# Optimization experiments

Hardware: AMD Instinct MI355X
Metric: run time of the kernel (lower is better)

Reference implementation:

```python
import jax, jax.numpy as jnp
import numpy as np

B = 32; H = 56; W = 56; C = 384; WS = 7; SHIFT = 3; NH = 12; HID = 1536; RANK = 192
N = WS * WS
NWIN = (H // WS) * (W // WS)


def _rel_index():
    coords = np.stack(np.meshgrid(np.arange(WS), np.arange(WS), indexing='ij')).reshape(2, -1)
    rel = (coords[:, :, None] - coords[:, None, :]).transpose(1, 2, 0)
    rel[..., 0] += WS - 1
    rel[..., 1] += WS - 1
    rel[..., 0] *= 2 * WS - 1
    return jnp.asarray(rel.sum(-1).reshape(-1))  # (N*N,) int


def _attn_mask():
    img = np.zeros((H, W))
    cnt = 0
    sls = (slice(0, -WS), slice(-WS, -SHIFT), slice(-SHIFT, None))
    for hs in sls:
        for ws_ in sls:
            img[hs, ws_] = cnt
            cnt += 1
    mw = img.reshape(H // WS, WS, W // WS, WS).transpose(0, 2, 1, 3).reshape(-1, N)
    am = mw[:, None, :] - mw[:, :, None]
    return jnp.asarray(np.where(am != 0, -100.0, 0.0).astype(np.float32))  # (nW,N,N)


REL_IDX = _rel_index()
ATTN_MASK = _attn_mask()


def _ln(x, g, b):
    m = x.mean(-1, keepdims=True)
    v = ((x - m) ** 2).mean(-1, keepdims=True)
    return (x - m) / jnp.sqrt(v + 1e-5) * g + b


def _flin(x, v, u, b):
    # FactorizedLinear: x @ V^T @ U^T + b
    return (x @ v.T) @ u.T + b


def setup_inputs() -> dict:
    key = jax.random.key(0)
    ks = jax.random.split(key, 12)
    def n(k, shape, s):
        return jax.random.normal(k, shape, jnp.float32) * s
    return {
        'x': jax.random.normal(ks[0], (B, H * W, C), jnp.float32),
        'norm1_g': jnp.ones((C,), jnp.float32), 'norm1_b': jnp.zeros((C,), jnp.float32),
        'rpb_table': n(ks[1], ((2 * WS - 1) ** 2, NH), 0.02),
        'qkv_v': n(ks[2], (RANK, C), 0.05), 'qkv_u': n(ks[3], (3 * C, RANK), 0.05),
        'qkv_b': jnp.zeros((3 * C,), jnp.float32),
        'proj_v': n(ks[4], (RANK, C), 0.05), 'proj_u': n(ks[5], (C, RANK), 0.05),
        'proj_b': jnp.zeros((C,), jnp.float32),
        'norm2_g': jnp.ones((C,), jnp.float32), 'norm2_b': jnp.zeros((C,), jnp.float32),
        'fc1_v': n(ks[6], (RANK, C), 0.05), 'fc1_u': n(ks[7], (HID, RANK), 0.05),
        'fc1_b': jnp.zeros((HID,), jnp.float32),
        'fc2_v': n(ks[8], (RANK, HID), 0.05), 'fc2_u': n(ks[9], (C, RANK), 0.05),
        'fc2_b': jnp.zeros((C,), jnp.float32),
    }


def reference(x, norm1_g, norm1_b, rpb_table, qkv_v, qkv_u, qkv_b,
              proj_v, proj_u, proj_b, norm2_g, norm2_b,
              fc1_v, fc1_u, fc1_b, fc2_v, fc2_u, fc2_b):
    hd = C // NH
    scale = hd ** -0.5
    shortcut = x
    y = _ln(x, norm1_g, norm1_b).reshape(B, H, W, C)
    y = jnp.roll(y, (-SHIFT, -SHIFT), axis=(1, 2))  # cyclic shift
    # window partition -> (B*nW, N, C)
    y = y.reshape(B, H // WS, WS, W // WS, WS, C).transpose(0, 1, 3, 2, 4, 5).reshape(-1, N, C)
    qkv = _flin(y, qkv_v, qkv_u, qkv_b).reshape(-1, N, 3, NH, hd).transpose(2, 0, 3, 1, 4)
    q, k, v = qkv[0] * scale, qkv[1], qkv[2]  # (B*nW, NH, N, hd)
    attn = jnp.einsum('bhnd,bhmd->bhnm', q, k)
    rpb = rpb_table[REL_IDX].reshape(N, N, NH).transpose(2, 0, 1)  # (NH,N,N)
    attn = attn + rpb[None]
    attn = attn.reshape(B, NWIN, NH, N, N) + ATTN_MASK[None, :, None]
    attn = jax.nn.softmax(attn, axis=-1).reshape(-1, NH, N, N)
    o = jnp.einsum('bhnm,bhmd->bhnd', attn, v).transpose(0, 2, 1, 3).reshape(-1, N, C)
    o = _flin(o, proj_v, proj_u, proj_b)
    # window reverse + reverse shift
    o = o.reshape(B, H // WS, W // WS, WS, WS, C).transpose(0, 1, 3, 2, 4, 5).reshape(B, H, W, C)
    o = jnp.roll(o, (SHIFT, SHIFT), axis=(1, 2)).reshape(B, H * W, C)
    x = shortcut + o
    z = _ln(x, norm2_g, norm2_b)
    z = jax.nn.gelu(_flin(z, fc1_v, fc1_u, fc1_b), approximate=False)
    z = _flin(z, fc2_v, fc2_u, fc2_b)
    return x + z
```

## Files before the change

### kernel.cpp

```cpp
#include <hip/hip_runtime.h>
#include <hip/hip_bf16.h>

using bf16 = __hip_bfloat16;
typedef __bf16 bf16x8 __attribute__((ext_vector_type(8)));
typedef float f32x4 __attribute__((ext_vector_type(4)));

#define MROWS 100352

__device__ __forceinline__ void async16(void* l, const void* g) {
    void* gg = const_cast<void*>(g);
    __builtin_amdgcn_global_load_lds((__attribute__((address_space(1))) void*)gg,
                                     (__attribute__((address_space(3))) void*)l, 16, 0, 0);
}

__device__ __forceinline__ float gelu_f(float x) {
    float u = 0.7978845608028654f * (x + 0.044715f * x * x * x);
    float e = __expf(2.0f * u);
    float t = 1.0f - 2.0f / (e + 1.0f);
    return 0.5f * x * (1.0f + t);
}

__device__ __forceinline__ unsigned short bfu(float x) {
    bf16 b = __float2bfloat16(x);
    union { bf16 b; unsigned short u; } c; c.b = b; return c.u;
}

struct Cvt8 { const float* s[8]; bf16* d[8]; int n[8]; };

__global__ __launch_bounds__(256) void cvt8_k(Cvt8 c) {
    int seg = blockIdx.y;
    int i4 = (blockIdx.x * 256 + threadIdx.x) * 4;
    if (i4 < c.n[seg]) {
        float4 v = *(const float4*)(c.s[seg] + i4);
        bf16* d = c.d[seg] + i4;
        d[0] = __float2bfloat16(v.x);
        d[1] = __float2bfloat16(v.y);
        d[2] = __float2bfloat16(v.z);
        d[3] = __float2bfloat16(v.w);
    }
}

__global__ __launch_bounds__(256) void ln1_window_k(const float* __restrict__ x,
                                                    const float* __restrict__ g,
                                                    const float* __restrict__ bta,
                                                    bf16* __restrict__ ywin) {
    int wrow = blockIdx.x * 4 + (threadIdx.x >> 6);
    int lane = threadIdx.x & 63;
    int tok = wrow % 49, win = wrow / 49;
    int i = tok / 7, j = tok % 7;
    int wwi = win & 7, whi = (win >> 3) & 7, bi = win >> 6;
    int hs = (whi * 7 + i + 3) % 56;
    int ws_ = (wwi * 7 + j + 3) % 56;
    const float* xr = x + ((size_t)bi * 3136 + (size_t)hs * 56 + ws_) * 384;
    float v[6]; float s = 0.f, s2 = 0.f;
#pragma unroll
    for (int u = 0; u < 6; ++u) { float t = xr[lane + 64 * u]; v[u] = t; s += t; s2 += t * t; }
#pragma unroll
    for (int d = 1; d < 64; d <<= 1) { s += __shfl_xor(s, d); s2 += __shfl_xor(s2, d); }
    float mean = s * (1.0f / 384.0f);
    float var = s2 * (1.0f / 384.0f) - mean * mean;
    float rstd = rsqrtf(var + 1e-5f);
    bf16* yr = ywin + (size_t)wrow * 384;
#pragma unroll
    for (int u = 0; u < 6; ++u) {
        int c = lane + 64 * u;
        yr[c] = __float2bfloat16((v[u] - mean) * rstd * g[c] + bta[c]);
    }
}

__global__ __launch_bounds__(256) void resid_ln2_k(const float* __restrict__ x,
                                                   const bf16* __restrict__ proj,
                                                   const float* __restrict__ g,
                                                   const float* __restrict__ bta,
                                                   float* __restrict__ x2,
                                                   bf16* __restrict__ z) {
    int row = blockIdx.x * 4 + (threadIdx.x >> 6);
    int lane = threadIdx.x & 63;
    int bi = row / 3136; int hw = row % 3136;
    int h = hw / 56, w = hw % 56;
    int h2 = (h + 53) % 56, w2 = (w + 53) % 56;
    int prow = ((bi * 8 + h2 / 7) * 8 + w2 / 7) * 49 + (h2 % 7) * 7 + (w2 % 7);
    const float* xr = x + (size_t)row * 384;
    const bf16* pr = proj + (size_t)prow * 384;
    float* x2r = x2 + (size_t)row * 384;
    float v[6]; float s = 0.f, s2 = 0.f;
#pragma unroll
    for (int u = 0; u < 6; ++u) {
        int c = lane + 64 * u;
        float t = xr[c] + __bfloat162float(pr[c]);
        v[u] = t; s += t; s2 += t * t;
        x2r[c] = t;
    }
#pragma unroll
    for (int d = 1; d < 64; d <<= 1) { s += __shfl_xor(s, d); s2 += __shfl_xor(s2, d); }
    float mean = s * (1.0f / 384.0f);
    float var = s2 * (1.0f / 384.0f) - mean * mean;
    float rstd = rsqrtf(var + 1e-5f);
    bf16* zr = z + (size_t)row * 384;
#pragma unroll
    for (int u = 0; u < 6; ++u) {
        int c = lane + 64 * u;
        zr[c] = __float2bfloat16((v[u] - mean) * rstd * g[c] + bta[c]);
    }
}

__global__ __launch_bounds__(256) void attn_mfma_k(const bf16* __restrict__ qkv,
                                                   const float* __restrict__ rpbt,
                                                   bf16* __restrict__ o) {
    __shared__ __align__(16) __bf16 vt_s[4][32 * 72];
    __shared__ __align__(16) __bf16 p_s[4][32 * 72];
    __shared__ float rpb_sh[676];
    const int win = blockIdx.x;
    const int r = blockIdx.y;
    const int wave = threadIdx.x >> 6, lane = threadIdx.x & 63;
    const int lo = lane & 15, hi = lane >> 4;
    const int whi = (win >> 3) & 7, wwi = win & 7;
    const bool bH = (whi == 7), bW = (wwi == 7);
    const bool boundary = bH || bW;
    __bf16* vt_w = vt_s[wave];
    __bf16* p_w = p_s[wave];
    const int h = r * 4 + wave;
    const bf16* qbase = qkv + (size_t)win * 49 * 1152 + h * 32;
    bf16x8 zf = {};

    for (int idx = threadIdx.x; idx < 676; idx += 256)
        rpb_sh[idx] = rpbt[(idx >> 2) * 12 + r * 4 + (idx & 3)];
    __syncthreads();

    {
        int m = lane;
        bf16x8 vrow[4];
#pragma unroll
        for (int d8 = 0; d8 < 4; ++d8)
            vrow[d8] = (m < 49) ? *(const bf16x8*)(qbase + (size_t)m * 1152 + 768 + d8 * 8) : zf;
#pragma unroll
        for (int d8 = 0; d8 < 4; ++d8)
#pragma unroll
            for (int e = 0; e < 8; ++e)
                vt_w[(d8 * 8 + e) * 72 + m] = vrow[d8][e];
    }
    bf16x8 aq[4], bk[4];
    const int kq = hi * 8;
#pragma unroll
    for (int ta = 0; ta < 4; ++ta) {
        int n = ta * 16 + lo;
        aq[ta] = (n < 49) ? *(const bf16x8*)(qbase + (size_t)n * 1152 + kq) : zf;
        bk[ta] = (n < 49) ? *(const bf16x8*)(qbase + (size_t)n * 1152 + 384 + kq) : zf;
    }
    f32x4 acc[4][4] = {};
#pragma unroll
    for (int ta = 0; ta < 4; ++ta)
#pragma unroll
        for (int tb = 0; tb < 4; ++tb)
            acc[ta][tb] = __builtin_amdgcn_mfma_f32_16x16x32_bf16(aq[ta], bk[tb], acc[ta][tb], 0, 0, 0);
    int i2[4], j2[4], rm[4];
#pragma unroll
    for (int tb = 0; tb < 4; ++tb) {
        int m = tb * 16 + lo;
        int mm = m < 49 ? m : 0;
        i2[tb] = mm / 7; j2[tb] = mm % 7;
        rm[tb] = (bH ? (i2[tb] < 4 ? 1 : 2) : 0) * 3 + (bW ? (j2[tb] < 4 ? 1 : 2) : 0);
    }
#pragma unroll
    for (int ta = 0; ta < 4; ++ta) {
#pragma unroll
        for (int j = 0; j < 4; ++j) {
            int n = ta * 16 + hi * 4 + j;
            int nn = n < 49 ? n : 0;
            int i1 = nn / 7, j1 = nn % 7;
            int rn = (bH ? (i1 < 4 ? 1 : 2) : 0) * 3 + (bW ? (j1 < 4 ? 1 : 2) : 0);
#pragma unroll
            for (int tb = 0; tb < 4; ++tb) {
                int m = tb * 16 + lo;
                float v;
                if (n < 49 && m < 49) {
                    v = acc[ta][tb][j] * 0.17677669529663687f
                        + rpb_sh[((i1 - i2[tb] + 6) * 13 + (j1 - j2[tb] + 6)) * 4 + wave];
                    if (boundary && rn != rm[tb]) v -= 100.0f;
                } else {
                    v = -1e30f;
                }
                acc[ta][tb][j] = v;
            }
        }
    }
    bf16x8 vb[2][2];
#pragma unroll
    for (int kb = 0; kb < 2; ++kb)
#pragma unroll
        for (int tb = 0; tb < 2; ++tb)
            vb[kb][tb] = *(const bf16x8*)(vt_w + (tb * 16 + lo) * 72 + kb * 32 + hi * 8);

    f32x4 oacc[4][2] = {};
#pragma unroll
    for (int half = 0; half < 2; ++half) {
#pragma unroll
        for (int tq = 0; tq < 2; ++tq) {
            int ta = half * 2 + tq;
#pragma unroll
            for (int j = 0; j < 4; ++j) {
                float mx = fmaxf(fmaxf(acc[ta][0][j], acc[ta][1][j]),
                                 fmaxf(acc[ta][2][j], acc[ta][3][j]));
                mx = fmaxf(mx, __shfl_xor(mx, 1));
                mx = fmaxf(mx, __shfl_xor(mx, 2));
                mx = fmaxf(mx, __shfl_xor(mx, 4));
                mx = fmaxf(mx, __shfl_xor(mx, 8));
                float e0 = __expf(acc[ta][0][j] - mx);
                float e1 = __expf(acc[ta][1][j] - mx);
                float e2 = __expf(acc[ta][2][j] - mx);
                float e3 = __expf(acc[ta][3][j] - mx);
                float sm = e0 + e1 + e2 + e3;
                sm += __shfl_xor(sm, 1);
                sm += __shfl_xor(sm, 2);
                sm += __shfl_xor(sm, 4);
                sm += __shfl_xor(sm, 8);
                float inv = 1.0f / sm;
                int nl = tq * 16 + hi * 4 + j;
                p_w[nl * 72 + lo]      = (__bf16)(e0 * inv);
                p_w[nl * 72 + 16 + lo] = (__bf16)(e1 * inv);
                p_w[nl * 72 + 32 + lo] = (__bf16)(e2 * inv);
                p_w[nl * 72 + 48 + lo] = (__bf16)(e3 * inv);
            }
        }
#pragma unroll
        for (int kb = 0; kb < 2; ++kb) {
#pragma unroll
            for (int tq = 0; tq < 2; ++tq) {
                bf16x8 pa = *(const bf16x8*)(p_w + (tq * 16 + lo) * 72 + kb * 32 + hi * 8);
#pragma unroll
                for (int tb = 0; tb < 2; ++tb)
                    oacc[half * 2 + tq][tb] =
                        __builtin_amdgcn_mfma_f32_16x16x32_bf16(pa, vb[kb][tb], oacc[half * 2 + tq][tb], 0, 0, 0);
            }
        }
    }
    bf16* obase = o + (size_t)win * 49 * 384 + h * 32;
#pragma unroll
    for (int ta = 0; ta < 4; ++ta) {
#pragma unroll
        for (int j = 0; j < 4; ++j) {
            int n = ta * 16 + hi * 4 + j;
            if (n < 49) {
#pragma unroll
                for (int tb = 0; tb < 2; ++tb)
                    obase[(size_t)n * 384 + tb * 16 + lo] = __float2bfloat16(oacc[ta][tb][j]);
            }
        }
    }
}

template <int K, int EPI>
__global__ __launch_bounds__(256) void gemm_bt(const bf16* __restrict__ A,
                                               const bf16* __restrict__ W,
                                               const float* __restrict__ bias,
                                               void* __restrict__ Cout,
                                               int N) {
    __shared__ __align__(16) bf16 lds_a[128 * 64];
    __shared__ __align__(16) bf16 lds_b[64 * 64];
    const int t = threadIdx.x;
    const int wave = t >> 6, lane = t & 63;
    const int gdx = gridDim.x;
    int flat = blockIdx.y * gdx + blockIdx.x;
    int q = (gdx * gridDim.y) >> 3;
    int work = (flat & 7) * q + (flat >> 3);
    const int n0 = (work % gdx) * 64, m0 = (work / gdx) * 128;
    const int wm = wave >> 1, wn = wave & 1;
    const int fr = lane & 15, hi = lane >> 4;
    f32x4 acc[4][2] = {};
    for (int kt = 0; kt < K; kt += 64) {
        if (kt > 0) __syncthreads();
#pragma unroll
        for (int i = 0; i < 4; ++i) {
            int u = i * 256 + t;
            int row = u >> 3, slot = u & 7;
            int gslot = slot ^ (row & 7);
            async16((char*)lds_a + u * 16, A + (size_t)(m0 + row) * K + kt + gslot * 8);
        }
#pragma unroll
        for (int i = 0; i < 2; ++i) {
            int u = i * 256 + t;
            int row = u >> 3, slot = u & 7;
            int gslot = slot ^ (row & 7);
            async16((char*)lds_b + u * 16, W + (size_t)(n0 + row) * K + kt + gslot * 8);
        }
        __syncthreads();
#pragma unroll
        for (int ks = 0; ks < 2; ++ks) {
            bf16x8 af[4], bfr[2];
#pragma unroll
            for (int mi = 0; mi < 4; ++mi) {
                int row = wm * 64 + mi * 16 + fr;
                int slot = (ks * 4 + hi) ^ (row & 7);
                af[mi] = *(const bf16x8*)((const char*)lds_a + row * 128 + slot * 16);
            }
#pragma unroll
            for (int ni = 0; ni < 2; ++ni) {
                int row = wn * 32 + ni * 16 + fr;
                int slot = (ks * 4 + hi) ^ (row & 7);
                bfr[ni] = *(const bf16x8*)((const char*)lds_b + row * 128 + slot * 16);
            }
#pragma unroll
            for (int mi = 0; mi < 4; ++mi)
#pragma unroll
                for (int ni = 0; ni < 2; ++ni)
                    acc[mi][ni] = __builtin_amdgcn_mfma_f32_16x16x32_bf16(bfr[ni], af[mi], acc[mi][ni], 0, 0, 0);
        }
    }
    const int rq4 = hi * 4;
#pragma unroll
    for (int mi = 0; mi < 4; ++mi) {
        int m = m0 + wm * 64 + mi * 16 + fr;
        size_t rowb = (size_t)m * N;
#pragma unroll
        for (int ni = 0; ni < 2; ++ni) {
            int nb = n0 + wn * 32 + ni * 16 + rq4;
            float v0 = acc[mi][ni][0], v1 = acc[mi][ni][1];
            float v2 = acc[mi][ni][2], v3 = acc[mi][ni][3];
            if (bias) {
                float4 b4 = *(const float4*)(bias + nb);
                v0 += b4.x; v1 += b4.y; v2 += b4.z; v3 += b4.w;
            }
            if (EPI == 1) { v0 = gelu_f(v0); v1 = gelu_f(v1); v2 = gelu_f(v2); v3 = gelu_f(v3); }
            if (EPI == 2) {
                float4* p = (float4*)((float*)Cout + rowb + nb);
                float4 o = *p;
                o.x += v0; o.y += v1; o.z += v2; o.w += v3;
                *p = o;
            } else {
                uint2 st;
                st.x = (unsigned)bfu(v0) | ((unsigned)bfu(v1) << 16);
                st.y = (unsigned)bfu(v2) | ((unsigned)bfu(v3) << 16);
                *(uint2*)((bf16*)Cout + rowb + nb) = st;
            }
        }
    }
}

extern "C" void kernel_launch(void* const* d_in, const int* in_sizes, int n_in,
                              void* d_out, int out_size, void* d_ws, size_t ws_size,
                              hipStream_t stream) {
    const float* x      = (const float*)d_in[0];
    const float* n1g    = (const float*)d_in[1];
    const float* n1b    = (const float*)d_in[2];
    const float* rpbt   = (const float*)d_in[3];
    const float* qkv_v  = (const float*)d_in[4];
    const float* qkv_u  = (const float*)d_in[5];
    const float* qkv_b  = (const float*)d_in[6];
    const float* proj_v = (const float*)d_in[7];
    const float* proj_u = (const float*)d_in[8];
    const float* proj_b = (const float*)d_in[9];
    const float* n2g    = (const float*)d_in[10];
    const float* n2b    = (const float*)d_in[11];
    const float* fc1_v  = (const float*)d_in[12];
    const float* fc1_u  = (const float*)d_in[13];
    const float* fc1_b  = (const float*)d_in[14];
    const float* fc2_v  = (const float*)d_in[15];
    const float* fc2_u  = (const float*)d_in[16];
    const float* fc2_b  = (const float*)d_in[17];

    char* ws = (char*)d_ws;
    bf16* wb = (bf16*)ws;
    bf16* w_qkv_v  = wb;
    bf16* w_qkv_u  = wb + 73728;
    bf16* w_proj_v = wb + 294912;
    bf16* w_proj_u = wb + 368640;
    bf16* w_fc1_v  = wb + 442368;
    bf16* w_fc1_u  = wb + 516096;
    bf16* w_fc2_v  = wb + 811008;
    bf16* w_fc2_u  = wb + 1105920;
    size_t off = (size_t)4 << 20;
    bf16* R1 = (bf16*)(ws + off); off += (size_t)MROWS * 1536 * 2;
    bf16* R2 = (bf16*)(ws + off); off += (size_t)MROWS * 384 * 2;
    bf16* R3 = (bf16*)(ws + off);
    float* out = (float*)d_out;

    Cvt8 c;
    c.s[0] = qkv_v;  c.d[0] = w_qkv_v;  c.n[0] = 73728;
    c.s[1] = qkv_u;  c.d[1] = w_qkv_u;  c.n[1] = 221184;
    c.s[2] = proj_v; c.d[2] = w_proj_v; c.n[2] = 73728;
    c.s[3] = proj_u; c.d[3] = w_proj_u; c.n[3] = 73728;
    c.s[4] = fc1_v;  c.d[4] = w_fc1_v;  c.n[4] = 73728;
    c.s[5] = fc1_u;  c.d[5] = w_fc1_u;  c.n[5] = 294912;
    c.s[6] = fc2_v;  c.d[6] = w_fc2_v;  c.n[6] = 294912;
    c.s[7] = fc2_u;  c.d[7] = w_fc2_u;  c.n[7] = 73728;
    cvt8_k<<<dim3(288, 8), 256, 0, stream>>>(c);

    ln1_window_k<<<MROWS / 4, 256, 0, stream>>>(x, n1g, n1b, R2);
    gemm_bt<384, 0><<<dim3(3, 784), 256, 0, stream>>>(R2, w_qkv_v, nullptr, R3, 192);
    gemm_bt<192, 0><<<dim3(18, 784), 256, 0, stream>>>(R3, w_qkv_u, qkv_b, R1, 1152);
    attn_mfma_k<<<dim3(2048, 3), 256, 0, stream>>>(R1, rpbt, R2);
    gemm_bt<384, 0><<<dim3(3, 784), 256, 0, stream>>>(R2, w_proj_v, nullptr, R3, 192);
    gemm_bt<192, 0><<<dim3(6, 784), 256, 0, stream>>>(R3, w_proj_u, proj_b, R1, 384);
    resid_ln2_k<<<MROWS / 4, 256, 0, stream>>>(x, R1, n2g, n2b, out, R2);
    gemm_bt<384, 0><<<dim3(3, 784), 256, 0, stream>>>(R2, w_fc1_v, nullptr, R3, 192);
    gemm_bt<192, 1><<<dim3(24, 784), 256, 0, stream>>>(R3, w_fc1_u, fc1_b, R1, 1536);
    gemm_bt<1536, 0><<<dim3(3, 784), 256, 0, stream>>>(R1, w_fc2_v, nullptr, R3, 192);
    gemm_bt<192, 2><<<dim3(6, 784), 256, 0, stream>>>(R3, w_fc2_u, fc2_b, out, 384);
}
```

Before: 900.5 us.

## Widen GEMM tiles to 64 columns per wave and cover full rank width

The GEMM kernel is generalized so that each wave computes a 64x64 output tile, with a configurable number of waves along N. The rank-192 down-projections now use a 128x192 block with 384 threads, so each A row-block is loaded once instead of three times. The up-projections use 128x128 blocks. This cuts redundant A-tile global loads and raises MFMA work per LDS fragment read, at the cost of more accumulator registers and fewer blocks in the grid.

```diff
diff --git a/kernel.cpp b/kernel.cpp
--- a/kernel.cpp
+++ b/kernel.cpp
@@ -249,44 +249,50 @@
     }
 }
 
-template <int K, int EPI>
-__global__ __launch_bounds__(256) void gemm_bt(const bf16* __restrict__ A,
-                                               const bf16* __restrict__ W,
-                                               const float* __restrict__ bias,
-                                               void* __restrict__ Cout,
-                                               int N) {
+template <int K, int NWN, int EPI>
+__global__ __launch_bounds__(NWN * 128) void gemm_w64(const bf16* __restrict__ A,
+                                                      const bf16* __restrict__ W,
+                                                      const float* __restrict__ bias,
+                                                      void* __restrict__ Cout,
+                                                      int N) {
+    constexpr int T = NWN * 128;
+    constexpr int BN = NWN * 64;
     __shared__ __align__(16) bf16 lds_a[128 * 64];
-    __shared__ __align__(16) bf16 lds_b[64 * 64];
+    __shared__ __align__(16) bf16 lds_b[BN * 64];
     const int t = threadIdx.x;
     const int wave = t >> 6, lane = t & 63;
+    const int wm = wave / NWN, wn = wave % NWN;
+    const int fr = lane & 15, hi = lane >> 4;
     const int gdx = gridDim.x;
     int flat = blockIdx.y * gdx + blockIdx.x;
     int q = (gdx * gridDim.y) >> 3;
     int work = (flat & 7) * q + (flat >> 3);
-    const int n0 = (work % gdx) * 64, m0 = (work / gdx) * 128;
-    const int wm = wave >> 1, wn = wave & 1;
-    const int fr = lane & 15, hi = lane >> 4;
-    f32x4 acc[4][2] = {};
+    const int n0 = (work % gdx) * BN, m0 = (work / gdx) * 128;
+    f32x4 acc[4][4] = {};
     for (int kt = 0; kt < K; kt += 64) {
         if (kt > 0) __syncthreads();
 #pragma unroll
-        for (int i = 0; i < 4; ++i) {
-            int u = i * 256 + t;
-            int row = u >> 3, slot = u & 7;
-            int gslot = slot ^ (row & 7);
-            async16((char*)lds_a + u * 16, A + (size_t)(m0 + row) * K + kt + gslot * 8);
-        }
-#pragma unroll
-        for (int i = 0; i < 2; ++i) {
-            int u = i * 256 + t;
-            int row = u >> 3, slot = u & 7;
-            int gslot = slot ^ (row & 7);
-            async16((char*)lds_b + u * 16, W + (size_t)(n0 + row) * K + kt + gslot * 8);
+        for (int i = 0; i < 1024; i += T) {
+            int u = i + t;
+            if (u < 1024) {
+                int row = u >> 3, slot = u & 7;
+                int gslot = slot ^ (row & 7);
+                async16((char*)lds_a + u * 16, A + (size_t)(m0 + row) * K + kt + gslot * 8);
+            }
+        }
+#pragma unroll
+        for (int i = 0; i < BN * 8; i += T) {
+            int u = i + t;
+            if (u < BN * 8) {
+                int row = u >> 3, slot = u & 7;
+                int gslot = slot ^ (row & 7);
+                async16((char*)lds_b + u * 16, W + (size_t)(n0 + row) * K + kt + gslot * 8);
+            }
         }
         __syncthreads();
 #pragma unroll
         for (int ks = 0; ks < 2; ++ks) {
-            bf16x8 af[4], bfr[2];
+            bf16x8 af[4], bfr[4];
 #pragma unroll
             for (int mi = 0; mi < 4; ++mi) {
                 int row = wm * 64 + mi * 16 + fr;
@@ -294,26 +300,25 @@
                 af[mi] = *(const bf16x8*)((const char*)lds_a + row * 128 + slot * 16);
             }
 #pragma unroll
-            for (int ni = 0; ni < 2; ++ni) {
-                int row = wn * 32 + ni * 16 + fr;
+            for (int ni = 0; ni < 4; ++ni) {
+                int row = wn * 64 + ni * 16 + fr;
                 int slot = (ks * 4 + hi) ^ (row & 7);
                 bfr[ni] = *(const bf16x8*)((const char*)lds_b + row * 128 + slot * 16);
             }
 #pragma unroll
             for (int mi = 0; mi < 4; ++mi)
 #pragma unroll
-                for (int ni = 0; ni < 2; ++ni)
+                for (int ni = 0; ni < 4; ++ni)
                     acc[mi][ni] = __builtin_amdgcn_mfma_f32_16x16x32_bf16(bfr[ni], af[mi], acc[mi][ni], 0, 0, 0);
         }
     }
-    const int rq4 = hi * 4;
 #pragma unroll
     for (int mi = 0; mi < 4; ++mi) {
         int m = m0 + wm * 64 + mi * 16 + fr;
         size_t rowb = (size_t)m * N;
 #pragma unroll
-        for (int ni = 0; ni < 2; ++ni) {
-            int nb = n0 + wn * 32 + ni * 16 + rq4;
+        for (int ni = 0; ni < 4; ++ni) {
+            int nb = n0 + wn * 64 + ni * 16 + hi * 4;
             float v0 = acc[mi][ni][0], v1 = acc[mi][ni][1];
             float v2 = acc[mi][ni][2], v3 = acc[mi][ni][3];
             if (bias) {
@@ -386,14 +391,14 @@
     cvt8_k<<<dim3(288, 8), 256, 0, stream>>>(c);
 
     ln1_window_k<<<MROWS / 4, 256, 0, stream>>>(x, n1g, n1b, R2);
-    gemm_bt<384, 0><<<dim3(3, 784), 256, 0, stream>>>(R2, w_qkv_v, nullptr, R3, 192);
-    gemm_bt<192, 0><<<dim3(18, 784), 256, 0, stream>>>(R3, w_qkv_u, qkv_b, R1, 1152);
+    gemm_w64<384, 3, 0><<<dim3(1, 784), 384, 0, stream>>>(R2, w_qkv_v, nullptr, R3, 192);
+    gemm_w64<192, 2, 0><<<dim3(9, 784), 256, 0, stream>>>(R3, w_qkv_u, qkv_b, R1, 1152);
     attn_mfma_k<<<dim3(2048, 3), 256, 0, stream>>>(R1, rpbt, R2);
-    gemm_bt<384, 0><<<dim3(3, 784), 256, 0, stream>>>(R2, w_proj_v, nullptr, R3, 192);
-    gemm_bt<192, 0><<<dim3(6, 784), 256, 0, stream>>>(R3, w_proj_u, proj_b, R1, 384);
+    gemm_w64<384, 3, 0><<<dim3(1, 784), 384, 0, stream>>>(R2, w_proj_v, nullptr, R3, 192);
+    gemm_w64<192, 2, 0><<<dim3(3, 784), 256, 0, stream>>>(R3, w_proj_u, proj_b, R1, 384);
     resid_ln2_k<<<MROWS / 4, 256, 0, stream>>>(x, R1, n2g, n2b, out, R2);
-    gemm_bt<384, 0><<<dim3(3, 784), 256, 0, stream>>>(R2, w_fc1_v, nullptr, R3, 192);
-    gemm_bt<192, 1><<<dim3(24, 784), 256, 0, stream>>>(R3, w_fc1_u, fc1_b, R1, 1536);
-    gemm_bt<1536, 0><<<dim3(3, 784), 256, 0, stream>>>(R1, w_fc2_v, nullptr, R3, 192);
-    gemm_bt<192, 2><<<dim3(6, 784), 256, 0, stream>>>(R3, w_fc2_u, fc2_b, out, 384);
-}
+    gemm_w64<384, 3, 0><<<dim3(1, 784), 384, 0, stream>>>(R2, w_fc1_v, nullptr, R3, 192);
+    gemm_w64<192, 2, 1><<<dim3(12, 784), 256, 0, stream>>>(R3, w_fc1_u, fc1_b, R1, 1536);
+    gemm_w64<1536, 3, 0><<<dim3(1, 784), 384, 0, stream>>>(R1, w_fc2_v, nullptr, R3, 192);
+    gemm_w64<192, 2, 2><<<dim3(3, 784), 256, 0, stream>>>(R3, w_fc2_u, fc2_b, out, 384);
+}
```

New measurement: 1.011 ms. 1.12x slower.

## Add persistent-B GEMM for K=192 up-projections with register-resident weights

Applied to the files above, without the earlier changes.

Adds a new GEMM kernel for the K=192 factorized up-projections. Each workgroup keeps its 128-column weight slice in registers and loops over eight 64-row A tiles, double-buffering them in LDS through async global-to-LDS loads with an XOR swizzle. Work is remapped across XCDs so neighbouring tiles land on the same die. This removes repeated weight loads per tile and overlaps A loads with MFMA work, at the cost of higher register pressure and fewer workgroups (grid shrinks fourfold in M).

```diff
diff --git a/kernel.cpp b/kernel.cpp
--- a/kernel.cpp
+++ b/kernel.cpp
@@ -336,6 +336,102 @@
     }
 }
 
+template <int N, int EPI>
+__global__ __launch_bounds__(256) void gemm_pb(const bf16* __restrict__ A,
+                                               const bf16* __restrict__ W,
+                                               const float* __restrict__ bias,
+                                               void* __restrict__ Cout) {
+    constexpr int K = 192;
+    constexpr int MT = 8;
+    __shared__ __align__(16) bf16 lds_a[2][64 * 192];
+    const int t = threadIdx.x;
+    const int wv = t >> 6, lane = t & 63;
+    const int fr = lane & 15, hi = lane >> 4;
+    const int gdx = gridDim.x;
+    int nwg = gdx * gridDim.y;
+    int flat = blockIdx.y * gdx + blockIdx.x;
+    int q = nwg >> 3, r = nwg & 7;
+    int xcd = flat & 7, sub = flat >> 3;
+    int work = (xcd < r ? xcd * (q + 1) : r * (q + 1) + (xcd - r) * q) + sub;
+    const int n0 = (work % gdx) * 128;
+    const int mstrip = (work / gdx) * (MT * 64);
+
+    bf16x8 breg[6][2];
+#pragma unroll
+    for (int kk = 0; kk < 6; ++kk)
+#pragma unroll
+        for (int nn = 0; nn < 2; ++nn)
+            breg[kk][nn] = *(const bf16x8*)(W + (size_t)(n0 + wv * 32 + nn * 16 + fr) * K + kk * 32 + hi * 8);
+
+    bf16* cur = (bf16*)lds_a[0];
+    bf16* nxt = (bf16*)lds_a[1];
+#pragma unroll
+    for (int i = 0; i < 6; ++i) {
+        int u = i * 256 + t;
+        int row = u / 24, slot = u % 24;
+        int gslot = slot ^ (row & 7);
+        async16((char*)cur + u * 16, A + (size_t)(mstrip + row) * K + gslot * 8);
+    }
+    __syncthreads();
+    for (int mt = 0; mt < MT; ++mt) {
+        if (mt + 1 < MT) {
+#pragma unroll
+            for (int i = 0; i < 6; ++i) {
+                int u = i * 256 + t;
+                int row = u / 24, slot = u % 24;
+                int gslot = slot ^ (row & 7);
+                async16((char*)nxt + u * 16,
+                        A + (size_t)(mstrip + (mt + 1) * 64 + row) * K + gslot * 8);
+            }
+        }
+        f32x4 acc[4][2] = {};
+#pragma unroll
+        for (int kk = 0; kk < 6; ++kk) {
+            bf16x8 af[4];
+#pragma unroll
+            for (int mi = 0; mi < 4; ++mi) {
+                int row = mi * 16 + fr;
+                int slot = (kk * 4 + hi) ^ (row & 7);
+                af[mi] = *(const bf16x8*)((const char*)cur + row * 384 + slot * 16);
+            }
+#pragma unroll
+            for (int mi = 0; mi < 4; ++mi)
+#pragma unroll
+                for (int nn = 0; nn < 2; ++nn)
+                    acc[mi][nn] = __builtin_amdgcn_mfma_f32_16x16x32_bf16(breg[kk][nn], af[mi], acc[mi][nn], 0, 0, 0);
+        }
+#pragma unroll
+        for (int mi = 0; mi < 4; ++mi) {
+            int m = mstrip + mt * 64 + mi * 16 + fr;
+            size_t rowb = (size_t)m * N;
+#pragma unroll
+            for (int nn = 0; nn < 2; ++nn) {
+                int nb = n0 + wv * 32 + nn * 16 + hi * 4;
+                float v0 = acc[mi][nn][0], v1 = acc[mi][nn][1];
+                float v2 = acc[mi][nn][2], v3 = acc[mi][nn][3];
+                if (bias) {
+                    float4 b4 = *(const float4*)(bias + nb);
+                    v0 += b4.x; v1 += b4.y; v2 += b4.z; v3 += b4.w;
+                }
+                if (EPI == 1) { v0 = gelu_f(v0); v1 = gelu_f(v1); v2 = gelu_f(v2); v3 = gelu_f(v3); }
+                if (EPI == 2) {
+                    float4* p = (float4*)((float*)Cout + rowb + nb);
+                    float4 o = *p;
+                    o.x += v0; o.y += v1; o.z += v2; o.w += v3;
+                    *p = o;
+                } else {
+                    uint2 st;
+                    st.x = (unsigned)bfu(v0) | ((unsigned)bfu(v1) << 16);
+                    st.y = (unsigned)bfu(v2) | ((unsigned)bfu(v3) << 16);
+                    *(uint2*)((bf16*)Cout + rowb + nb) = st;
+                }
+            }
+        }
+        __syncthreads();
+        bf16* tmp = cur; cur = nxt; nxt = tmp;
+    }
+}
+
 extern "C" void kernel_launch(void* const* d_in, const int* in_sizes, int n_in,
                               void* d_out, int out_size, void* d_ws, size_t ws_size,
                               hipStream_t stream) {
@@ -387,13 +483,13 @@
 
     ln1_window_k<<<MROWS / 4, 256, 0, stream>>>(x, n1g, n1b, R2);
     gemm_bt<384, 0><<<dim3(3, 784), 256, 0, stream>>>(R2, w_qkv_v, nullptr, R3, 192);
-    gemm_bt<192, 0><<<dim3(18, 784), 256, 0, stream>>>(R3, w_qkv_u, qkv_b, R1, 1152);
+    gemm_pb<1152, 0><<<dim3(9, 196), 256, 0, stream>>>(R3, w_qkv_u, qkv_b, R1);
     attn_mfma_k<<<dim3(2048, 3), 256, 0, stream>>>(R1, rpbt, R2);
     gemm_bt<384, 0><<<dim3(3, 784), 256, 0, stream>>>(R2, w_proj_v, nullptr, R3, 192);
-    gemm_bt<192, 0><<<dim3(6, 784), 256, 0, stream>>>(R3, w_proj_u, proj_b, R1, 384);
+    gemm_pb<384, 0><<<dim3(3, 196), 256, 0, stream>>>(R3, w_proj_u, proj_b, R1);
     resid_ln2_k<<<MROWS / 4, 256, 0, stream>>>(x, R1, n2g, n2b, out, R2);
     gemm_bt<384, 0><<<dim3(3, 784), 256, 0, stream>>>(R2, w_fc1_v, nullptr, R3, 192);
-    gemm_bt<192, 1><<<dim3(24, 784), 256, 0, stream>>>(R3, w_fc1_u, fc1_b, R1, 1536);
+    gemm_pb<1536, 1><<<dim3(12, 196), 256, 0, stream>>>(R3, w_fc1_u, fc1_b, R1);
     gemm_bt<1536, 0><<<dim3(3, 784), 256, 0, stream>>>(R1, w_fc2_v, nullptr, R3, 192);
-    gemm_bt<192, 2><<<dim3(6, 784), 256, 0, stream>>>(R3, w_fc2_u, fc2_b, out, 384);
-}
+    gemm_pb<384, 2><<<dim3(3, 196), 256, 0, stream>>>(R3, w_fc2_u, fc2_b, out);
+}
```

New measurement: 926.4 us. 2.9% more time.

## Precompute attention bias+mask tiles per window type; simplify GEMM load addressing

Applied to the files above, without the earlier changes.

Adds a small kernel that precomputes, for each of the four window boundary types and twelve heads, the relative-position bias plus shift mask laid out in MFMA accumulator order. The attention kernel then reads one float4 per row group instead of computing indices, gathering from LDS and applying masks, which also removes an LDS table and a block barrier. Separately, the GEMM hoists its async-load address math out of the k loop and adds a minimum-occupancy launch bound of 6. The new 192 KB bias buffer is read from global/L2 by every attention block.

```diff
diff --git a/kernel.cpp b/kernel.cpp
--- a/kernel.cpp
+++ b/kernel.cpp
@@ -37,6 +37,37 @@
         d[1] = __float2bfloat16(v.y);
         d[2] = __float2bfloat16(v.z);
         d[3] = __float2bfloat16(v.w);
+    }
+}
+
+__global__ __launch_bounds__(256) void bias_pre_k(const float* __restrict__ rpbt,
+                                                  float* __restrict__ biasf) {
+    int wt = blockIdx.x / 12, h = blockIdx.x % 12;
+    int t = threadIdx.x;
+    int lane = t >> 2, tb = t & 3;
+    int hi = lane >> 4, lo = lane & 15;
+    int m = tb * 16 + lo;
+    bool bH = (wt & 2) != 0, bW = (wt & 1) != 0;
+    float* outb = biasf + (size_t)blockIdx.x * 4096;
+    int mm = m < 49 ? m : 0;
+    int i2 = mm / 7, j2 = mm % 7;
+    int rm = (bH ? (i2 < 4 ? 1 : 2) : 0) * 3 + (bW ? (j2 < 4 ? 1 : 2) : 0);
+#pragma unroll
+    for (int ta = 0; ta < 4; ++ta) {
+#pragma unroll
+        for (int j = 0; j < 4; ++j) {
+            int n = ta * 16 + hi * 4 + j;
+            float v;
+            if (n < 49 && m < 49) {
+                int i1 = n / 7, j1 = n % 7;
+                int rn = (bH ? (i1 < 4 ? 1 : 2) : 0) * 3 + (bW ? (j1 < 4 ? 1 : 2) : 0);
+                v = rpbt[((i1 - i2 + 6) * 13 + (j1 - j2 + 6)) * 12 + h];
+                if (rn != rm) v -= 100.0f;
+            } else {
+                v = -1e30f;
+            }
+            outb[(ta * 4 + j) * 256 + t] = v;
+        }
     }
 }
 
@@ -105,27 +136,22 @@
 }
 
 __global__ __launch_bounds__(256) void attn_mfma_k(const bf16* __restrict__ qkv,
-                                                   const float* __restrict__ rpbt,
+                                                   const float* __restrict__ biasf,
                                                    bf16* __restrict__ o) {
     __shared__ __align__(16) __bf16 vt_s[4][32 * 72];
     __shared__ __align__(16) __bf16 p_s[4][32 * 72];
-    __shared__ float rpb_sh[676];
     const int win = blockIdx.x;
     const int r = blockIdx.y;
     const int wave = threadIdx.x >> 6, lane = threadIdx.x & 63;
     const int lo = lane & 15, hi = lane >> 4;
     const int whi = (win >> 3) & 7, wwi = win & 7;
-    const bool bH = (whi == 7), bW = (wwi == 7);
-    const bool boundary = bH || bW;
+    const int wt = ((whi == 7) ? 2 : 0) + ((wwi == 7) ? 1 : 0);
     __bf16* vt_w = vt_s[wave];
     __bf16* p_w = p_s[wave];
     const int h = r * 4 + wave;
     const bf16* qbase = qkv + (size_t)win * 49 * 1152 + h * 32;
+    const float* btile = biasf + (size_t)(wt * 12 + h) * 4096;
     bf16x8 zf = {};
-
-    for (int idx = threadIdx.x; idx < 676; idx += 256)
-        rpb_sh[idx] = rpbt[(idx >> 2) * 12 + r * 4 + (idx & 3)];
-    __syncthreads();
 
     {
         int m = lane;
@@ -153,35 +179,15 @@
 #pragma unroll
         for (int tb = 0; tb < 4; ++tb)
             acc[ta][tb] = __builtin_amdgcn_mfma_f32_16x16x32_bf16(aq[ta], bk[tb], acc[ta][tb], 0, 0, 0);
-    int i2[4], j2[4], rm[4];
-#pragma unroll
-    for (int tb = 0; tb < 4; ++tb) {
-        int m = tb * 16 + lo;
-        int mm = m < 49 ? m : 0;
-        i2[tb] = mm / 7; j2[tb] = mm % 7;
-        rm[tb] = (bH ? (i2[tb] < 4 ? 1 : 2) : 0) * 3 + (bW ? (j2[tb] < 4 ? 1 : 2) : 0);
-    }
 #pragma unroll
     for (int ta = 0; ta < 4; ++ta) {
 #pragma unroll
         for (int j = 0; j < 4; ++j) {
-            int n = ta * 16 + hi * 4 + j;
-            int nn = n < 49 ? n : 0;
-            int i1 = nn / 7, j1 = nn % 7;
-            int rn = (bH ? (i1 < 4 ? 1 : 2) : 0) * 3 + (bW ? (j1 < 4 ? 1 : 2) : 0);
-#pragma unroll
-            for (int tb = 0; tb < 4; ++tb) {
-                int m = tb * 16 + lo;
-                float v;
-                if (n < 49 && m < 49) {
-                    v = acc[ta][tb][j] * 0.17677669529663687f
-                        + rpb_sh[((i1 - i2[tb] + 6) * 13 + (j1 - j2[tb] + 6)) * 4 + wave];
-                    if (boundary && rn != rm[tb]) v -= 100.0f;
-                } else {
-                    v = -1e30f;
-                }
-                acc[ta][tb][j] = v;
-            }
+            float4 b4 = *(const float4*)(btile + (ta * 4 + j) * 256 + lane * 4);
+            acc[ta][0][j] = fmaf(acc[ta][0][j], 0.17677669529663687f, b4.x);
+            acc[ta][1][j] = fmaf(acc[ta][1][j], 0.17677669529663687f, b4.y);
+            acc[ta][2][j] = fmaf(acc[ta][2][j], 0.17677669529663687f, b4.z);
+            acc[ta][3][j] = fmaf(acc[ta][3][j], 0.17677669529663687f, b4.w);
         }
     }
     bf16x8 vb[2][2];
@@ -250,11 +256,11 @@
 }
 
 template <int K, int EPI>
-__global__ __launch_bounds__(256) void gemm_bt(const bf16* __restrict__ A,
-                                               const bf16* __restrict__ W,
-                                               const float* __restrict__ bias,
-                                               void* __restrict__ Cout,
-                                               int N) {
+__global__ __launch_bounds__(256, 6) void gemm_bt(const bf16* __restrict__ A,
+                                                  const bf16* __restrict__ W,
+                                                  const float* __restrict__ bias,
+                                                  void* __restrict__ Cout,
+                                                  int N) {
     __shared__ __align__(16) bf16 lds_a[128 * 64];
     __shared__ __align__(16) bf16 lds_b[64 * 64];
     const int t = threadIdx.x;
@@ -266,23 +272,21 @@
     const int n0 = (work % gdx) * 64, m0 = (work / gdx) * 128;
     const int wm = wave >> 1, wn = wave & 1;
     const int fr = lane & 15, hi = lane >> 4;
+    const int srow = t >> 3;
+    const int gslot = (t & 7) ^ (srow & 7);
+    const bf16* abase = A + (size_t)(m0 + srow) * K + gslot * 8;
+    const bf16* bbase = W + (size_t)(n0 + srow) * K + gslot * 8;
+    char* la = (char*)lds_a + t * 16;
+    char* lb = (char*)lds_b + t * 16;
     f32x4 acc[4][2] = {};
     for (int kt = 0; kt < K; kt += 64) {
         if (kt > 0) __syncthreads();
 #pragma unroll
-        for (int i = 0; i < 4; ++i) {
-            int u = i * 256 + t;
-            int row = u >> 3, slot = u & 7;
-            int gslot = slot ^ (row & 7);
-            async16((char*)lds_a + u * 16, A + (size_t)(m0 + row) * K + kt + gslot * 8);
-        }
-#pragma unroll
-        for (int i = 0; i < 2; ++i) {
-            int u = i * 256 + t;
-            int row = u >> 3, slot = u & 7;
-            int gslot = slot ^ (row & 7);
-            async16((char*)lds_b + u * 16, W + (size_t)(n0 + row) * K + kt + gslot * 8);
-        }
+        for (int i = 0; i < 4; ++i)
+            async16(la + i * 4096, abase + (size_t)i * 32 * K + kt);
+#pragma unroll
+        for (int i = 0; i < 2; ++i)
+            async16(lb + i * 4096, bbase + (size_t)i * 32 * K + kt);
         __syncthreads();
 #pragma unroll
         for (int ks = 0; ks < 2; ++ks) {
@@ -368,6 +372,7 @@
     bf16* w_fc1_u  = wb + 516096;
     bf16* w_fc2_v  = wb + 811008;
     bf16* w_fc2_u  = wb + 1105920;
+    float* biasf   = (float*)(ws + 3145728);
     size_t off = (size_t)4 << 20;
     bf16* R1 = (bf16*)(ws + off); off += (size_t)MROWS * 1536 * 2;
     bf16* R2 = (bf16*)(ws + off); off += (size_t)MROWS * 384 * 2;
@@ -384,11 +389,12 @@
     c.s[6] = fc2_v;  c.d[6] = w_fc2_v;  c.n[6] = 294912;
     c.s[7] = fc2_u;  c.d[7] = w_fc2_u;  c.n[7] = 73728;
     cvt8_k<<<dim3(288, 8), 256, 0, stream>>>(c);
+    bias_pre_k<<<48, 256, 0, stream>>>(rpbt, biasf);
 
     ln1_window_k<<<MROWS / 4, 256, 0, stream>>>(x, n1g, n1b, R2);
     gemm_bt<384, 0><<<dim3(3, 784), 256, 0, stream>>>(R2, w_qkv_v, nullptr, R3, 192);
     gemm_bt<192, 0><<<dim3(18, 784), 256, 0, stream>>>(R3, w_qkv_u, qkv_b, R1, 1152);
-    attn_mfma_k<<<dim3(2048, 3), 256, 0, stream>>>(R1, rpbt, R2);
+    attn_mfma_k<<<dim3(2048, 3), 256, 0, stream>>>(R1, biasf, R2);
     gemm_bt<384, 0><<<dim3(3, 784), 256, 0, stream>>>(R2, w_proj_v, nullptr, R3, 192);
     gemm_bt<192, 0><<<dim3(6, 784), 256, 0, stream>>>(R3, w_proj_u, proj_b, R1, 384);
     resid_ln2_k<<<MROWS / 4, 256, 0, stream>>>(x, R1, n2g, n2b, out, R2);
```

Result: faster. 858.2 us (-4.7%).
